# Optimization experiments

Hardware: AMD Instinct MI355X
Metric: run time of the kernel (lower is better)

## Reference

```python
import jax, jax.numpy as jnp
import numpy as np
from jax import lax

N, T, D, W, H, V = 256, 64, 1280, 256, 512, 10000
NULL_IDX = 0  # ignore_index


def setup_inputs() -> dict:
    key = jax.random.key(0)
    ks = jax.random.split(key, 9)
    features = jax.random.normal(ks[0], (N, D), dtype=jnp.float32)
    captions = jax.random.randint(ks[1], (N, T + 1), 0, V, dtype=jnp.int64)
    # learned parameters
    W_proj = jax.random.normal(ks[2], (D, H), dtype=jnp.float32) / np.sqrt(D)
    b_proj = jnp.zeros((H,), dtype=jnp.float32)
    W_embed = jax.random.normal(ks[3], (V, W), dtype=jnp.float32) / np.sqrt(V)
    Wx = jax.random.normal(ks[4], (W, H), dtype=jnp.float32) / np.sqrt(W)
    Wh = jax.random.normal(ks[5], (H, H), dtype=jnp.float32) / np.sqrt(H)
    b = jnp.zeros((H,), dtype=jnp.float32)
    W_out = jax.random.normal(ks[6], (H, V), dtype=jnp.float32) / np.sqrt(H)
    b_out = jnp.zeros((V,), dtype=jnp.float32)
    return {"features": features, "captions": captions, "W_proj": W_proj,
            "b_proj": b_proj, "W_embed": W_embed, "Wx": Wx, "Wh": Wh, "b": b,
            "W_out": W_out, "b_out": b_out}


def reference(features, captions, W_proj, b_proj, W_embed, Wx, Wh, b, W_out, b_out):
    captions_in = captions[:, :-1]   # (N, T)
    captions_out = captions[:, 1:]   # (N, T)

    h0 = features @ W_proj + b_proj                      # (N, H)
    x = W_embed[captions_in]                             # (N, T, W)
    # Precompute input-to-hidden part; recurrence only needs h @ Wh.
    xWxb = jnp.einsum('ntw,wh->nth', x, Wx) + b          # (N, T, H)

    def step(h_prev, xt):
        h_next = jnp.tanh(h_prev @ Wh + xt)
        return h_next, h_next

    _, hs = lax.scan(step, h0, jnp.swapaxes(xWxb, 0, 1))  # (T, N, H)
    h = jnp.swapaxes(hs, 0, 1)                            # (N, T, H)

    scores = jnp.einsum('nth,hv->ntv', h, W_out) + b_out  # (N, T, V)
    logp = jax.nn.log_softmax(scores, axis=-1)
    nll = -jnp.take_along_axis(logp, captions_out[..., None], axis=-1)[..., 0]
    mask = (captions_out != NULL_IDX).astype(nll.dtype)
    loss = jnp.sum(nll * mask) / N
    return loss
```

## Files before the change

kernel.cpp:

```cpp
#include <hip/hip_runtime.h>
#include <hip/hip_bf16.h>
#include <hip/hip_fp8.h>

#define NB 256
#define TT 64
#define DD 1280
#define WW 256
#define HH 512
#define VV 10000
#define VP 10112
#define NCT 79
#define MROWS (NB*TT)

typedef short short8 __attribute__((ext_vector_type(8)));
typedef float f32x4 __attribute__((ext_vector_type(4)));
typedef int   int4v __attribute__((ext_vector_type(4)));
typedef int   int8v __attribute__((ext_vector_type(8)));

static __device__ __forceinline__ unsigned short f2bf(float x){
    unsigned int u = __float_as_uint(x);
    unsigned int r = u + 0x7FFFu + ((u >> 16) & 1u);
    return (unsigned short)(r >> 16);
}
static __device__ __forceinline__ float bf2f(unsigned short u){
    return __uint_as_float(((unsigned int)u) << 16);
}
static __device__ __forceinline__ unsigned char f2f8(float x){
    __hip_fp8_e4m3 q(x);
    return (unsigned char)q.__x;
}
static __device__ __forceinline__ float f82f(unsigned char b){
    __hip_fp8_e4m3 q; q.__x = b;
    return (float)q;
}
static __device__ __forceinline__ unsigned enc4(float x){
    unsigned s = (x < 0.f) ? 8u : 0u;
    float a = fabsf(x);
    unsigned m;
    if      (a < 0.25f) m = 0;
    else if (a < 0.75f) m = 1;
    else if (a < 1.25f) m = 2;
    else if (a < 1.75f) m = 3;
    else if (a < 2.5f)  m = 4;
    else if (a < 3.5f)  m = 5;
    else if (a < 5.0f)  m = 6;
    else                m = 7;
    return s | m;
}
static __device__ __forceinline__ void gload16b(const unsigned char* g, unsigned char* l){
    __builtin_amdgcn_global_load_lds(
        (const __attribute__((address_space(1))) void*)g,
        (__attribute__((address_space(3))) void*)l, 16, 0, 0);
}


__global__ __launch_bounds__(256) void k_prep(const float* __restrict__ feat,
                                              const float* __restrict__ W_proj,
                                              const float* __restrict__ bp,
                                              float* __restrict__ h0,
                                              const float* __restrict__ Wx,
                                              unsigned short* __restrict__ WxT,
                                              const float* __restrict__ Wh,
                                              unsigned char* __restrict__ WhT4,
                                              const float* __restrict__ W_out,
                                              unsigned char* __restrict__ WoT8p,
                                              const float* __restrict__ bo,
                                              float* __restrict__ bop){
    __shared__ unsigned short tileS[64][17];
    __shared__ float fs[DD];
    int b = blockIdx.x;
    int tid = threadIdx.x;
    if (b < 256){
        int n = b;
        for (int i = tid; i < DD; i += 256) fs[i] = feat[(size_t)n*DD + i];
        __syncthreads();
        int c0 = tid, c1 = tid + 256;
        float a0 = 0.f, a1 = 0.f;
        for (int d = 0; d < DD; ++d){
            float fv = fs[d];
            a0 += fv * W_proj[(size_t)d*HH + c0];
            a1 += fv * W_proj[(size_t)d*HH + c1];
        }
        h0[(size_t)n*HH + c0] = a0 + bp[c0];
        h0[(size_t)n*HH + c1] = a1 + bp[c1];
    } else if (b < 384){
        int r = b - 256;
        int c0 = (r & 7)*64, r0 = (r >> 3)*16;
        int c = tid & 63, rr = tid >> 6;
        #pragma unroll
        for (int j = 0; j < 4; ++j){
            int rw_ = rr + j*4;
            tileS[c][rw_] = f2bf(Wx[(size_t)(r0+rw_)*HH + c0 + c]);
        }
        __syncthreads();
        int rw = tid & 15, cw = tid >> 4;
        #pragma unroll
        for (int j = 0; j < 4; ++j){
            int c2 = cw + j*16;
            WxT[(size_t)(c0+c2)*WW + r0 + rw] = tileS[c2][rw];
        }
    } else if (b < 896){
        int r = b - 384;
        int j = r >> 1;
        int col = (r & 1)*256 + tid;
        float w0 = Wh[(size_t)(2*j  )*HH + col] * 32.0f;
        float w1 = Wh[(size_t)(2*j+1)*HH + col] * 32.0f;
        WhT4[(size_t)col*256 + j] = (unsigned char)(enc4(w0) | (enc4(w1) << 4));
    } else if (b < 5952){
        unsigned char (*tileC)[20] = reinterpret_cast<unsigned char (*)[20]>(&tileS[0][0]);
        int r = b - 896;
        int c0 = (r % 158)*64, r0 = (r / 158)*16;
        int c = tid & 63, rr = tid >> 6;
        #pragma unroll
        for (int j = 0; j < 4; ++j){
            int rw_ = rr + j*4;
            unsigned char v = 0;
            if (c0 + c < VV) v = f2f8(W_out[(size_t)(r0+rw_)*VV + c0 + c]);
            tileC[c][rw_] = v;
        }
        __syncthreads();
        int rw = tid & 15, cw = tid >> 4;
        #pragma unroll
        for (int j = 0; j < 4; ++j){
            int c2 = cw + j*16;
            int col = c0 + c2, k = r0 + rw;
            if (col < VP){
                size_t addr = ((size_t)((col >> 7)*4 + (k >> 7)))*16384
                            + (unsigned)((col & 127)*128 + (k & 127));
                WoT8p[addr] = tileC[c2][rw];
            }
        }
    } else {
        int i = (b - 5952)*256 + tid;
        if (i < VP) bop[i] = (i < VV) ? bo[i]*1.44269504f : -30000.0f;
    }
}

__global__ __launch_bounds__(256) void k_e2(const float* __restrict__ We,
                                            const unsigned short* __restrict__ WxT,
                                            const float* __restrict__ bias,
                                            unsigned short* __restrict__ E2b){
    int lane = threadIdx.x & 63;
    int wv   = threadIdx.x >> 6;
    int l15 = lane & 15, lhi = lane >> 4;
    int rbase = blockIdx.x*64 + wv*16;
    int arow = rbase + l15; if (arow > VV-1) arow = VV-1;
    short8 a[8];
    #pragma unroll
    for (int kk = 0; kk < 8; ++kk){
        const float* src = We + (size_t)arow*WW + kk*32 + lhi*8;
        float4 g0 = *reinterpret_cast<const float4*>(src);
        float4 g1 = *reinterpret_cast<const float4*>(src + 4);
        short8 v;
        v[0]=(short)f2bf(g0.x); v[1]=(short)f2bf(g0.y); v[2]=(short)f2bf(g0.z); v[3]=(short)f2bf(g0.w);
        v[4]=(short)f2bf(g1.x); v[5]=(short)f2bf(g1.y); v[6]=(short)f2bf(g1.z); v[7]=(short)f2bf(g1.w);
        a[kk] = v;
    }
    int ct0 = blockIdx.y*8;
    for (int ct = ct0; ct < ct0+8; ++ct){
        int c0 = ct*16;
        f32x4 acc = {0.f,0.f,0.f,0.f};
        #pragma unroll
        for (int kk = 0; kk < 8; ++kk){
            short8 b = *reinterpret_cast<const short8*>(WxT + (size_t)(c0 + l15)*WW + kk*32 + lhi*8);
            acc = __builtin_amdgcn_mfma_f32_16x16x32_bf16(a[kk], b, acc, 0, 0, 0);
        }
        float bb = bias[c0 + l15];
        #pragma unroll
        for (int r = 0; r < 4; ++r){
            int row = rbase + lhi*4 + r;
            if (row < VV) E2b[(size_t)row*HH + c0 + l15] = f2bf(acc[r] + bb);
        }
    }
}

__global__ __launch_bounds__(512) void k_rnn(const float* __restrict__ h0,
                                             const unsigned char* __restrict__ WhT4,
                                             const unsigned short* __restrict__ E2b,
                                             const int* __restrict__ caps,
                                             unsigned char* __restrict__ hA8){
    __shared__ __align__(32) unsigned char hl[2][HH];
    int tid = threadIdx.x;
    int lane = tid & 63, wv = tid >> 6;
    int l15 = lane & 15, lhi = lane >> 4;
    int n = blockIdx.x;
    int c0w = wv*64;
    int mycol = c0w + lane;
    unsigned char* hbase = hA8 + ((size_t)((n>>1)*4 + (wv>>1)))*16384
                               + (unsigned)((n&1)*64*128 + (mycol & 127));

    int4v b[4][4];
    #pragma unroll
    for (int ct = 0; ct < 4; ++ct){
        int col = c0w + ct*16 + l15;
        #pragma unroll
        for (int kt = 0; kt < 4; ++kt){
            b[ct][kt] = *reinterpret_cast<const int4v*>(WhT4 + (size_t)col*256 + kt*64 + lhi*16);
            asm volatile("" : "+v"(b[ct][kt]));
        }
    }
    hl[0][tid] = f2f8(h0[(size_t)n*HH + tid]);
    __syncthreads();
    int cur = 0;
    const f32x4 z = {0.f,0.f,0.f,0.f};
    for (int t = 0; t < TT; ++t){
        int tok = caps[n*(TT+1) + t];
        unsigned short xv = E2b[(size_t)tok*HH + mycol];
        int8v a[4];
        #pragma unroll
        for (int kt = 0; kt < 4; ++kt)
            a[kt] = *reinterpret_cast<const int8v*>(&hl[cur][kt*128 + lhi*32]);
        f32x4 acc[4][4];
        #pragma unroll
        for (int ct = 0; ct < 4; ++ct)
            #pragma unroll
            for (int kt = 0; kt < 4; ++kt){
                int8v bb = __builtin_shufflevector(b[ct][kt], b[ct][kt], 0,1,2,3,0,1,2,3);
                acc[ct][kt] = __builtin_amdgcn_mfma_scale_f32_16x16x128_f8f6f4(
                    a[kt], bb, z,
                    0, 4,
                    0, (int)0x7F7F7F7F,
                    0, (int)0x7A7A7A7A);
            }
        float s0 = (acc[0][0][0] + acc[0][1][0]) + (acc[0][2][0] + acc[0][3][0]);
        float s1 = (acc[1][0][0] + acc[1][1][0]) + (acc[1][2][0] + acc[1][3][0]);
        float s2 = (acc[2][0][0] + acc[2][1][0]) + (acc[2][2][0] + acc[2][3][0]);
        float s3 = (acc[3][0][0] + acc[3][1][0]) + (acc[3][2][0] + acc[3][3][0]);
        float v = (lhi == 0) ? s0 : (lhi == 1) ? s1 : (lhi == 2) ? s2 : s3;
        float x = v + bf2f(xv);
        float e = __expf(2.f*x);
        float th = 1.f - 2.f/(e + 1.f);
        unsigned char hv = f2f8(th);
        hl[cur^1][mycol] = hv;
        hbase[t*128] = hv;
        __syncthreads();
        cur ^= 1;
    }
}

__global__ __launch_bounds__(512) void k_scores(const unsigned char* __restrict__ hA8,
                                                const unsigned char* __restrict__ WoT8p,
                                                const float* __restrict__ bop,
                                                float* __restrict__ pps){
    __shared__ unsigned char As[16384];
    __shared__ unsigned char Bs[16384];
    int bid = blockIdx.x;
    int x = bid & 7;
    int local = bid >> 3;
    int ct = local >> 4;
    int rt = x*16 + (local & 15);

    int tid = threadIdx.x;
    int lane = tid & 63, wv = tid >> 6;
    int l15 = lane & 15, lhi = lane >> 4;
    int wr = wv >> 1, wc = wv & 1;
    const unsigned char* Abase = hA8   + (size_t)rt*65536;
    const unsigned char* Bbase = WoT8p + (size_t)ct*65536;

    unsigned coff[2];
    #pragma unroll
    for (int i = 0; i < 2; ++i){
        unsigned chunk = (unsigned)(i*512 + tid);
        unsigned rowloc = chunk >> 3;
        coff[i] = rowloc*128 + (((chunk & 7u) ^ (rowloc & 7u))*16u);
    }

    f32x4 acc[2][4];
    #pragma unroll
    for (int m = 0; m < 2; ++m)
        #pragma unroll
        for (int n = 0; n < 4; ++n)
            acc[m][n] = (f32x4){0.f,0.f,0.f,0.f};

    for (int kt = 0; kt < 4; ++kt){
        #pragma unroll
        for (int i = 0; i < 2; ++i){
            gload16b(Abase + kt*16384 + coff[i], As + (unsigned)((i*512 + tid) * 16));
            gload16b(Bbase + kt*16384 + coff[i], Bs + (unsigned)((i*512 + tid) * 16));
        }
        __syncthreads();
        int8v af[2];
        #pragma unroll
        for (int m = 0; m < 2; ++m){
            unsigned row = (unsigned)(wr*32 + m*16 + l15);
            int4v c0 = *reinterpret_cast<const int4v*>(As + row*128 + (((unsigned)(lhi*2+0) ^ (row&7))*16));
            int4v c1 = *reinterpret_cast<const int4v*>(As + row*128 + (((unsigned)(lhi*2+1) ^ (row&7))*16));
            af[m] = __builtin_shufflevector(c0, c1, 0,1,2,3,4,5,6,7);
        }
        #pragma unroll
        for (int n = 0; n < 4; ++n){
            unsigned col = (unsigned)(wc*64 + n*16 + l15);
            int4v c0 = *reinterpret_cast<const int4v*>(Bs + col*128 + (((unsigned)(lhi*2+0) ^ (col&7))*16));
            int4v c1 = *reinterpret_cast<const int4v*>(Bs + col*128 + (((unsigned)(lhi*2+1) ^ (col&7))*16));
            int8v bf = __builtin_shufflevector(c0, c1, 0,1,2,3,4,5,6,7);
            #pragma unroll
            for (int m = 0; m < 2; ++m)
                acc[m][n] = __builtin_amdgcn_mfma_scale_f32_16x16x128_f8f6f4(
                    af[m], bf, acc[m][n],
                    0, 0,
                    0, (int)0x7F7F7F7F,
                    0, (int)0x7F7F7F7F);
        }
        __syncthreads();
    }

    const float LOG2E = 1.44269504f;
    float srun[2][4];
    #pragma unroll
    for (int m = 0; m < 2; ++m)
        #pragma unroll
        for (int r = 0; r < 4; ++r) srun[m][r] = 0.f;
    #pragma unroll
    for (int n = 0; n < 4; ++n){
        int colg = ct*128 + wc*64 + n*16 + l15;
        float bb2 = bop[colg];
        #pragma unroll
        for (int m = 0; m < 2; ++m)
            #pragma unroll
            for (int r = 0; r < 4; ++r)
                srun[m][r] += exp2f(fmaf(acc[m][n][r], LOG2E, bb2));
    }
    #pragma unroll
    for (int off = 1; off < 16; off <<= 1)
        #pragma unroll
        for (int m = 0; m < 2; ++m)
            #pragma unroll
            for (int r = 0; r < 4; ++r)
                srun[m][r] += __shfl_xor(srun[m][r], off, 64);
    float* red = (float*)As;
    if (wc == 1 && l15 == 0){
        #pragma unroll
        for (int m = 0; m < 2; ++m)
            #pragma unroll
            for (int r = 0; r < 4; ++r){
                int ri = wr*32 + m*16 + lhi*4 + r;
                red[ri] = srun[m][r];
            }
    }
    __syncthreads();
    if (wc == 0 && l15 == 0){
        #pragma unroll
        for (int m = 0; m < 2; ++m)
            #pragma unroll
            for (int r = 0; r < 4; ++r){
                int ri = wr*32 + m*16 + lhi*4 + r;
                int gr = rt*128 + ri;
                pps[(size_t)ct*MROWS + gr] = srun[m][r] + red[ri];
            }
    }
}

__global__ __launch_bounds__(256) void k_tsc(const unsigned char* __restrict__ hA8,
                                             const unsigned char* __restrict__ WoT8p,
                                             const float* __restrict__ bo,
                                             const int* __restrict__ caps,
                                             float* __restrict__ t0arr){
    int lane = threadIdx.x & 63, w = threadIdx.x >> 6;
    int row = blockIdx.x*4 + w;
    int tgt = caps[(row >> 6)*(TT+1) + (row & 63) + 1];
    int k0 = lane*8;
    int ktile = k0 >> 7, kin = k0 & 127;
    const unsigned char* hp = hA8   + ((size_t)((row >> 7)*4 + ktile))*16384
                                    + (unsigned)((row & 127)*128 + kin);
    const unsigned char* wp = WoT8p + ((size_t)((tgt >> 7)*4 + ktile))*16384
                                    + (unsigned)((tgt & 127)*128 + kin);
    float sum = 0.f;
    #pragma unroll
    for (int j = 0; j < 8; ++j)
        sum += f82f(hp[j]) * f82f(wp[j]);
    #pragma unroll
    for (int off = 1; off < 64; off <<= 1)
        sum += __shfl_xor(sum, off, 64);
    if (lane == 0) t0arr[row] = sum + bo[tgt];
}

__global__ __launch_bounds__(256) void k_loss1(const float* __restrict__ pps,
                                               const float* __restrict__ t0arr,
                                               const int* __restrict__ caps,
                                               float* __restrict__ bsum){
    __shared__ float reds[256];
    int tid = threadIdx.x;
    int rloc = tid & 63, q = tid >> 6;
    int row = blockIdx.x*64 + rloc;
    int c0 = q*20, c1 = (q == 3) ? NCT : c0 + 20;
    float s = 0.f;
    for (int ct = c0; ct < c1; ++ct)
        s += pps[(size_t)ct*MROWS + row];
    reds[tid] = s;
    __syncthreads();
    if (q == 0){
        s = reds[rloc] + reds[64+rloc] + reds[128+rloc] + reds[192+rloc];
        int tgt = caps[(row >> 6)*(TT+1) + (row & 63) + 1];
        reds[rloc] = (tgt != 0) ? (__logf(s) - t0arr[row]) : 0.f;
    }
    __syncthreads();
    if (tid < 32) reds[tid] += reds[tid+32];
    __syncthreads();
    if (tid < 16) reds[tid] += reds[tid+16];
    __syncthreads();
    if (tid < 8)  reds[tid] += reds[tid+8];
    __syncthreads();
    if (tid < 4)  reds[tid] += reds[tid+4];
    __syncthreads();
    if (tid == 0) bsum[blockIdx.x] = reds[0] + reds[1] + reds[2] + reds[3];
}

__global__ __launch_bounds__(64) void k_loss2(const float* __restrict__ bsum, float* __restrict__ out){
    __shared__ float red[64];
    int tid = threadIdx.x;
    red[tid] = bsum[tid] + bsum[tid+64] + bsum[tid+128] + bsum[tid+192];
    __syncthreads();
    for (int off = 32; off > 0; off >>= 1){
        if (tid < off) red[tid] += red[tid+off];
        __syncthreads();
    }
    if (tid == 0) out[0] = red[0] / (float)NB;
}

extern "C" void kernel_launch(void* const* d_in, const int* in_sizes, int n_in,
                              void* d_out, int out_size, void* d_ws, size_t ws_size,
                              hipStream_t stream) {
    const float* features = (const float*)d_in[0];
    const int*   captions = (const int*)  d_in[1];
    const float* W_proj   = (const float*)d_in[2];
    const float* b_proj   = (const float*)d_in[3];
    const float* W_embed  = (const float*)d_in[4];
    const float* Wx       = (const float*)d_in[5];
    const float* Wh       = (const float*)d_in[6];
    const float* b_       = (const float*)d_in[7];
    const float* W_out    = (const float*)d_in[8];
    const float* b_out    = (const float*)d_in[9];
    float* out = (float*)d_out;

    char* ws = (char*)d_ws;
    unsigned short* E2b   = (unsigned short*)(ws + 0);
    float*          h0    = (float*)         (ws + 10240000);
    unsigned char*  WhT4  = (unsigned char*) (ws + 10764288);
    unsigned short* WxT   = (unsigned short*)(ws + 10895360);
    unsigned char*  WoT8p = (unsigned char*) (ws + 11157504);
    float*          bop   = (float*)         (ws + 16334848);
    unsigned char*  hA8   = (unsigned char*) (ws + 16375296);
    float*          pps   = (float*)         (ws + 24763904);
    float*          t0arr = (float*)         (ws + 29941248);
    float*          bsum  = (float*)         (ws + 30006784);
    if (ws_size < 30007808u) return;

    k_prep<<<5992, 256, 0, stream>>>(features, W_proj, b_proj, h0,
                                     Wx, WxT, Wh, WhT4, W_out, WoT8p, b_out, bop);
    k_e2<<<dim3(157,4), 256, 0, stream>>>(W_embed, WxT, b_, E2b);
    k_rnn<<<NB, 512, 0, stream>>>(h0, WhT4, E2b, captions, hA8);
    k_scores<<<128*NCT, 512, 0, stream>>>(hA8, WoT8p, bop, pps);
    k_tsc<<<MROWS/4, 256, 0, stream>>>(hA8, WoT8p, b_out, captions, t0arr);
    k_loss1<<<256, 256, 0, stream>>>(pps, t0arr, captions, bsum);
    k_loss2<<<1, 64, 0, stream>>>(bsum, out);
}
```

Baseline: 295.0 us.

## Vectorize W_out transpose stores, prefetch RNN embeddings, fuse target-score into scores kernel

The W_out fp8 packing now has 64 threads each write one 16-byte row segment instead of scattering single bytes. The RNN loop prefetches the next timestep's token and embedding value so the dependent global load is off the recurrence's critical path. The separate target-logit kernel is folded into extra blocks of the scores launch, removing one kernel launch. The trade-offs are fewer active threads in the packing store, one more live register in the RNN loop, and extra tail blocks in the scores grid.

```diff
diff --git a/kernel.cpp b/kernel.cpp
--- a/kernel.cpp
+++ b/kernel.cpp
@@ -119,15 +119,14 @@
             tileC[c][rw_] = v;
         }
         __syncthreads();
-        int rw = tid & 15, cw = tid >> 4;
-        #pragma unroll
-        for (int j = 0; j < 4; ++j){
-            int c2 = cw + j*16;
-            int col = c0 + c2, k = r0 + rw;
+        if (tid < 64){
+            int col = c0 + tid;
             if (col < VP){
-                size_t addr = ((size_t)((col >> 7)*4 + (k >> 7)))*16384
-                            + (unsigned)((col & 127)*128 + (k & 127));
-                WoT8p[addr] = tileC[c2][rw];
+                const unsigned* src = reinterpret_cast<const unsigned*>(&tileC[tid][0]);
+                uint4 v = make_uint4(src[0], src[1], src[2], src[3]);
+                size_t addr = ((size_t)((col >> 7)*4 + (r0 >> 7)))*16384
+                            + (unsigned)((col & 127)*128 + (r0 & 127));
+                *reinterpret_cast<uint4*>(WoT8p + addr) = v;
             }
         }
     } else {
@@ -200,12 +199,14 @@
         }
     }
     hl[0][tid] = f2f8(h0[(size_t)n*HH + tid]);
+    unsigned short xv = E2b[(size_t)caps[n*(TT+1)]*HH + mycol];
     __syncthreads();
     int cur = 0;
     const f32x4 z = {0.f,0.f,0.f,0.f};
     for (int t = 0; t < TT; ++t){
-        int tok = caps[n*(TT+1) + t];
-        unsigned short xv = E2b[(size_t)tok*HH + mycol];
+        unsigned short xv_next = 0;
+        if (t + 1 < TT)
+            xv_next = E2b[(size_t)caps[n*(TT+1) + t + 1]*HH + mycol];
         int8v a[4];
         #pragma unroll
         for (int kt = 0; kt < 4; ++kt)
@@ -233,6 +234,7 @@
         unsigned char hv = f2f8(th);
         hl[cur^1][mycol] = hv;
         hbase[t*128] = hv;
+        xv = xv_next;
         __syncthreads();
         cur ^= 1;
     }
@@ -241,18 +243,41 @@
 __global__ __launch_bounds__(512) void k_scores(const unsigned char* __restrict__ hA8,
                                                 const unsigned char* __restrict__ WoT8p,
                                                 const float* __restrict__ bop,
+                                                const float* __restrict__ bo,
+                                                const int* __restrict__ caps,
+                                                float* __restrict__ t0arr,
                                                 float* __restrict__ pps){
     __shared__ unsigned char As[16384];
     __shared__ unsigned char Bs[16384];
     int bid = blockIdx.x;
+    int tid = threadIdx.x;
+    int lane = tid & 63, wv = tid >> 6;
+    int l15 = lane & 15, lhi = lane >> 4;
+
+    if (bid >= 128*NCT){
+        int row = (bid - 128*NCT)*8 + wv;
+        int tgt = caps[(row >> 6)*(TT+1) + (row & 63) + 1];
+        int k0 = lane*8;
+        int ktile = k0 >> 7, kin = k0 & 127;
+        const unsigned char* hp = hA8   + ((size_t)((row >> 7)*4 + ktile))*16384
+                                        + (unsigned)((row & 127)*128 + kin);
+        const unsigned char* wp = WoT8p + ((size_t)((tgt >> 7)*4 + ktile))*16384
+                                        + (unsigned)((tgt & 127)*128 + kin);
+        float sum = 0.f;
+        #pragma unroll
+        for (int j = 0; j < 8; ++j)
+            sum += f82f(hp[j]) * f82f(wp[j]);
+        #pragma unroll
+        for (int off = 1; off < 64; off <<= 1)
+            sum += __shfl_xor(sum, off, 64);
+        if (lane == 0) t0arr[row] = sum + bo[tgt];
+        return;
+    }
+
     int x = bid & 7;
     int local = bid >> 3;
     int ct = local >> 4;
     int rt = x*16 + (local & 15);
-
-    int tid = threadIdx.x;
-    int lane = tid & 63, wv = tid >> 6;
-    int l15 = lane & 15, lhi = lane >> 4;
     int wr = wv >> 1, wc = wv & 1;
     const unsigned char* Abase = hA8   + (size_t)rt*65536;
     const unsigned char* Bbase = WoT8p + (size_t)ct*65536;
@@ -348,30 +373,6 @@
                 pps[(size_t)ct*MROWS + gr] = srun[m][r] + red[ri];
             }
     }
-}
-
-__global__ __launch_bounds__(256) void k_tsc(const unsigned char* __restrict__ hA8,
-                                             const unsigned char* __restrict__ WoT8p,
-                                             const float* __restrict__ bo,
-                                             const int* __restrict__ caps,
-                                             float* __restrict__ t0arr){
-    int lane = threadIdx.x & 63, w = threadIdx.x >> 6;
-    int row = blockIdx.x*4 + w;
-    int tgt = caps[(row >> 6)*(TT+1) + (row & 63) + 1];
-    int k0 = lane*8;
-    int ktile = k0 >> 7, kin = k0 & 127;
-    const unsigned char* hp = hA8   + ((size_t)((row >> 7)*4 + ktile))*16384
-                                    + (unsigned)((row & 127)*128 + kin);
-    const unsigned char* wp = WoT8p + ((size_t)((tgt >> 7)*4 + ktile))*16384
-                                    + (unsigned)((tgt & 127)*128 + kin);
-    float sum = 0.f;
-    #pragma unroll
-    for (int j = 0; j < 8; ++j)
-        sum += f82f(hp[j]) * f82f(wp[j]);
-    #pragma unroll
-    for (int off = 1; off < 64; off <<= 1)
-        sum += __shfl_xor(sum, off, 64);
-    if (lane == 0) t0arr[row] = sum + bo[tgt];
 }
 
 __global__ __launch_bounds__(256) void k_loss1(const float* __restrict__ pps,
@@ -449,8 +450,7 @@
                                      Wx, WxT, Wh, WhT4, W_out, WoT8p, b_out, bop);
     k_e2<<<dim3(157,4), 256, 0, stream>>>(W_embed, WxT, b_, E2b);
     k_rnn<<<NB, 512, 0, stream>>>(h0, WhT4, E2b, captions, hA8);
-    k_scores<<<128*NCT, 512, 0, stream>>>(hA8, WoT8p, bop, pps);
-    k_tsc<<<MROWS/4, 256, 0, stream>>>(hA8, WoT8p, b_out, captions, t0arr);
+    k_scores<<<128*NCT + MROWS/8, 512, 0, stream>>>(hA8, WoT8p, bop, b_out, captions, t0arr, pps);
     k_loss1<<<256, 256, 0, stream>>>(pps, t0arr, captions, bsum);
     k_loss2<<<1, 64, 0, stream>>>(bsum, out);
 }
```

Result: faster. 286.6 us (-2.9%).
